# Optimization experiments

Hardware: AMD Instinct MI355X
Metric: run time of the kernel (lower is better)

Reference implementation:

```python
import jax, jax.numpy as jnp
import numpy as np

NEI_SIZE = [16]  # matches init kwarg nei_size

def setup_inputs() -> dict:
    key = jax.random.key(0)
    k = jax.random.split(key, 5)
    B, N, S = 512, 32, 16
    EF, NF = 64, 128
    return {
        "x": jax.random.normal(k[0], (B, N, NF), dtype=jnp.float32),
        "x_nei_rel": jax.random.normal(k[1], (B, N * S, EF), dtype=jnp.float32),
        "x_nei_node": jax.random.normal(k[2], (B, N * S, NF), dtype=jnp.float32),
        "W1_w": jax.random.normal(k[3], (NF, EF + NF), dtype=jnp.float32) * 0.05,
        "W1_b": jax.random.normal(k[4], (NF,), dtype=jnp.float32) * 0.05,
        "i": 0,
    }

def reference(x, x_nei_rel, x_nei_node, W1_w, W1_b, i):
    S = NEI_SIZE[i]                       # now_nei_size (static python int)
    B, N, D = x.shape                     # N = n_neibor, D = nodeFea
    norm = 1.0 / np.sqrt(D).astype(np.float32)
    # concat edge+node feats and project: [B, N*S, EF+NF] -> [B, N*S, D]
    x_nei = jnp.concatenate([x_nei_rel, x_nei_node], axis=-1)
    v = (x_nei @ W1_w.T + W1_b).reshape(B, N, S, D)
    # per-node attention over its S neighbors
    alpha = jnp.einsum('bnd,bnsd->bns', x, v) * norm   # [B, N, S]
    alpha = jax.nn.softmax(alpha, axis=-1)
    # weighted neighbor sum
    return jnp.einsum('bns,bnsd->bnd', alpha, v)       # [B, N, D]
```

## Files before the change

### kernel.cpp

```cpp
#include <hip/hip_runtime.h>
#include <stdint.h>


typedef __attribute__((ext_vector_type(8))) short short8;
typedef __attribute__((ext_vector_type(4))) float float4_t;
typedef __attribute__((ext_vector_type(4))) unsigned short ushort4_t;

#define GRID_ 1024
#define ITERS_ 16

__device__ __forceinline__ unsigned short f2bf(float f) {
    uint32_t u = __float_as_uint(f);
    u += 0x7fffu + ((u >> 16) & 1u);
    return (unsigned short)(u >> 16);
}

__device__ __forceinline__ int aoff(int s, int kc) {
    return (((kc >> 5) * 64) + (((kc & 31) >> 3) * 16) + s) * 8 + (kc & 7);
}

__global__ __launch_bounds__(256) void nei_attn_kernel(
    const float* __restrict__ x,
    const float* __restrict__ rel,
    const float* __restrict__ node,
    const float* __restrict__ W,
    const float* __restrict__ bias,
    float* __restrict__ out)
{
    __shared__ __align__(16) unsigned short lds_a[6 * 64 * 8];
    __shared__ float lds_x[128];
    __shared__ float lds_v[16 * 132];
    __shared__ float lds_ap[256];
    __shared__ float lds_alpha[16];

    const int t    = threadIdx.x;
    const int lane = t & 63;
    const int wv   = t >> 6;
    const int l15  = lane & 15;
    const int quad = lane >> 4;

    short8 bf0[6], bf1[6];
    const int row0 = wv * 32 + l15;
    const int row1 = row0 + 16;
    const float bias0 = bias[row0];
    const float bias1 = bias[row1];
    #pragma unroll
    for (int q = 0; q < 6; ++q) {
        const float* p0 = W + row0 * 192 + q * 32 + quad * 8;
        const float* p1 = W + row1 * 192 + q * 32 + quad * 8;
        float4_t a0 = *(const float4_t*)p0;
        float4_t a1 = *(const float4_t*)(p0 + 4);
        float4_t c0 = *(const float4_t*)p1;
        float4_t c1 = *(const float4_t*)(p1 + 4);
        short8 f0, f1;
        f0[0] = (short)f2bf(a0.x); f0[1] = (short)f2bf(a0.y);
        f0[2] = (short)f2bf(a0.z); f0[3] = (short)f2bf(a0.w);
        f0[4] = (short)f2bf(a1.x); f0[5] = (short)f2bf(a1.y);
        f0[6] = (short)f2bf(a1.z); f0[7] = (short)f2bf(a1.w);
        f1[0] = (short)f2bf(c0.x); f1[1] = (short)f2bf(c0.y);
        f1[2] = (short)f2bf(c0.z); f1[3] = (short)f2bf(c0.w);
        f1[4] = (short)f2bf(c1.x); f1[5] = (short)f2bf(c1.y);
        f1[6] = (short)f2bf(c1.z); f1[7] = (short)f2bf(c1.w);
        bf0[q] = f0; bf1[q] = f1;
    }

    const int s0 = t >> 4,       kc0 = (t & 15) << 2;
    const int s1 = t >> 5,       kc1 = 64 + ((t & 31) << 2);
    const int s2 = s1 + 8;
    const int ao0 = aoff(s0, kc0);
    const int ao1 = aoff(s1, kc1);
    const int ao2 = aoff(s2, kc1);

    int idx = blockIdx.x * ITERS_;

    float4_t pf0, pf1, pf2, pfx;
    {
        const float* pr = rel  + idx * 1024;
        const float* pn = node + idx * 2048;
        pf0 = *(const float4_t*)(pr + t * 4);
        pf1 = *(const float4_t*)(pn + t * 4);
        pf2 = *(const float4_t*)(pn + 1024 + t * 4);
        if (t < 32) pfx = *(const float4_t*)(x + idx * 128 + t * 4);
    }

    for (int it = 0; it < ITERS_; ++it) {
        {
            ushort4_t u;
            u[0] = f2bf(pf0.x); u[1] = f2bf(pf0.y); u[2] = f2bf(pf0.z); u[3] = f2bf(pf0.w);
            *(ushort4_t*)&lds_a[ao0] = u;
            u[0] = f2bf(pf1.x); u[1] = f2bf(pf1.y); u[2] = f2bf(pf1.z); u[3] = f2bf(pf1.w);
            *(ushort4_t*)&lds_a[ao1] = u;
            u[0] = f2bf(pf2.x); u[1] = f2bf(pf2.y); u[2] = f2bf(pf2.z); u[3] = f2bf(pf2.w);
            *(ushort4_t*)&lds_a[ao2] = u;
            if (t < 32) *(float4_t*)&lds_x[t * 4] = pfx;
        }
        __syncthreads();

        if (it + 1 < ITERS_) {
            const int nidx = idx + 1;
            const float* pr = rel  + nidx * 1024;
            const float* pn = node + nidx * 2048;
            pf0 = *(const float4_t*)(pr + t * 4);
            pf1 = *(const float4_t*)(pn + t * 4);
            pf2 = *(const float4_t*)(pn + 1024 + t * 4);
            if (t < 32) pfx = *(const float4_t*)(x + nidx * 128 + t * 4);
        }

        float4_t acc0 = {0.f, 0.f, 0.f, 0.f};
        float4_t acc1 = {0.f, 0.f, 0.f, 0.f};
        #pragma unroll
        for (int q = 0; q < 6; ++q) {
            short8 af = *(const short8*)&lds_a[(q * 64 + lane) * 8];
            acc0 = __builtin_amdgcn_mfma_f32_16x16x32_bf16(af, bf0[q], acc0, 0, 0, 0);
            acc1 = __builtin_amdgcn_mfma_f32_16x16x32_bf16(af, bf1[q], acc1, 0, 0, 0);
        }

        const int col0 = wv * 32 + l15;
        const int rb = quad * 4;
        #pragma unroll
        for (int r = 0; r < 4; ++r) {
            lds_v[(rb + r) * 132 + col0]      = acc0[r] + bias0;
            lds_v[(rb + r) * 132 + col0 + 16] = acc1[r] + bias1;
        }
        __syncthreads();

        {
            const int sA = t >> 4, dA = t & 15;
            float p = 0.f;
            #pragma unroll
            for (int j = 0; j < 8; ++j) {
                const int d = dA + (j << 4);
                p += lds_x[d] * lds_v[sA * 132 + d];
            }
            lds_ap[t] = p;
        }
        __syncthreads();

        if (t < 16) {
            float a = 0.f;
            #pragma unroll
            for (int j = 0; j < 16; ++j) a += lds_ap[t * 16 + j];
            lds_alpha[t] = a * 0.08838834764831845f;
        }
        __syncthreads();

        if (t < 128) {
            float m = lds_alpha[0];
            #pragma unroll
            for (int s = 1; s < 16; ++s) m = fmaxf(m, lds_alpha[s]);
            float e[16], den = 0.f;
            #pragma unroll
            for (int s = 0; s < 16; ++s) { e[s] = __expf(lds_alpha[s] - m); den += e[s]; }
            float o = 0.f;
            #pragma unroll
            for (int s = 0; s < 16; ++s) o += e[s] * lds_v[s * 132 + t];
            out[idx * 128 + t] = o / den;
        }
        ++idx;
    }
}

extern "C" void kernel_launch(void* const* d_in, const int* in_sizes, int n_in,
                              void* d_out, int out_size, void* d_ws, size_t ws_size,
                              hipStream_t stream) {
    const float* x    = (const float*)d_in[0];
    const float* rel  = (const float*)d_in[1];
    const float* node = (const float*)d_in[2];
    const float* W    = (const float*)d_in[3];
    const float* bias = (const float*)d_in[4];
    float* out = (float*)d_out;
    hipLaunchKernelGGL(nei_attn_kernel, dim3(GRID_), dim3(256), 0, stream,
                       x, rel, node, W, bias, out);
}
```

Measured before the change: 263.0 us.

## Give each wave its own node tile with W staged in LDS and shuffle softmax

Restructures the kernel so each of four waves independently processes whole (b,n) tiles: the full bf16 weight matrix is staged once in LDS and shared across waves. Each wave computes all 128 output columns with MFMA and does the attention dot product, softmax and weighted sum entirely in registers via cross-lane shuffles. This removes the per-iteration block-wide __syncthreads barriers and LDS round trips for v, alpha and partial sums. Grid and iterations change to 512 blocks x 4 waves x 8 tiles, with launch bounds hinting two blocks per CU. Costs are roughly 48KB of LDS per block, more LDS reads of W per tile and heavier register use for the prefetch buffers.

```diff
diff --git a/kernel.cpp b/kernel.cpp
--- a/kernel.cpp
+++ b/kernel.cpp
@@ -6,8 +6,8 @@
 typedef __attribute__((ext_vector_type(4))) float float4_t;
 typedef __attribute__((ext_vector_type(4))) unsigned short ushort4_t;
 
-#define GRID_ 1024
-#define ITERS_ 16
+#define NBLK 512
+#define ITERS 8
 
 __device__ __forceinline__ unsigned short f2bf(float f) {
     uint32_t u = __float_as_uint(f);
@@ -19,7 +19,7 @@
     return (((kc >> 5) * 64) + (((kc & 31) >> 3) * 16) + s) * 8 + (kc & 7);
 }
 
-__global__ __launch_bounds__(256) void nei_attn_kernel(
+__global__ __launch_bounds__(256, 2) void nei_attn_kernel(
     const float* __restrict__ x,
     const float* __restrict__ rel,
     const float* __restrict__ node,
@@ -27,11 +27,9 @@
     const float* __restrict__ bias,
     float* __restrict__ out)
 {
-    __shared__ __align__(16) unsigned short lds_a[6 * 64 * 8];
-    __shared__ float lds_x[128];
-    __shared__ float lds_v[16 * 132];
-    __shared__ float lds_ap[256];
-    __shared__ float lds_alpha[16];
+    __shared__ __align__(16) unsigned short lds_w[48 * 64 * 8];
+    __shared__ __align__(16) unsigned short lds_a[4][6 * 64 * 8];
+    __shared__ __align__(16) float lds_x[4][128];
 
     const int t    = threadIdx.x;
     const int lane = t & 63;
@@ -39,124 +37,137 @@
     const int l15  = lane & 15;
     const int quad = lane >> 4;
 
-    short8 bf0[6], bf1[6];
-    const int row0 = wv * 32 + l15;
-    const int row1 = row0 + 16;
-    const float bias0 = bias[row0];
-    const float bias1 = bias[row1];
     #pragma unroll
-    for (int q = 0; q < 6; ++q) {
-        const float* p0 = W + row0 * 192 + q * 32 + quad * 8;
-        const float* p1 = W + row1 * 192 + q * 32 + quad * 8;
-        float4_t a0 = *(const float4_t*)p0;
-        float4_t a1 = *(const float4_t*)(p0 + 4);
-        float4_t c0 = *(const float4_t*)p1;
-        float4_t c1 = *(const float4_t*)(p1 + 4);
-        short8 f0, f1;
-        f0[0] = (short)f2bf(a0.x); f0[1] = (short)f2bf(a0.y);
-        f0[2] = (short)f2bf(a0.z); f0[3] = (short)f2bf(a0.w);
-        f0[4] = (short)f2bf(a1.x); f0[5] = (short)f2bf(a1.y);
-        f0[6] = (short)f2bf(a1.z); f0[7] = (short)f2bf(a1.w);
-        f1[0] = (short)f2bf(c0.x); f1[1] = (short)f2bf(c0.y);
-        f1[2] = (short)f2bf(c0.z); f1[3] = (short)f2bf(c0.w);
-        f1[4] = (short)f2bf(c1.x); f1[5] = (short)f2bf(c1.y);
-        f1[6] = (short)f2bf(c1.z); f1[7] = (short)f2bf(c1.w);
-        bf0[q] = f0; bf1[q] = f1;
+    for (int c = 0; c < 12; ++c) {
+        const int ch = c * 4 + wv;
+        const int ct = ch / 6, q = ch - ct * 6;
+        const float* p = W + (ct * 16 + l15) * 192 + q * 32 + quad * 8;
+        float4_t w0 = *(const float4_t*)p;
+        float4_t w1 = *(const float4_t*)(p + 4);
+        short8 f;
+        f[0] = (short)f2bf(w0.x); f[1] = (short)f2bf(w0.y);
+        f[2] = (short)f2bf(w0.z); f[3] = (short)f2bf(w0.w);
+        f[4] = (short)f2bf(w1.x); f[5] = (short)f2bf(w1.y);
+        f[6] = (short)f2bf(w1.z); f[7] = (short)f2bf(w1.w);
+        *(short8*)&lds_w[(ch * 64 + lane) * 8] = f;
+    }
+    float bias_l[8];
+    #pragma unroll
+    for (int ct = 0; ct < 8; ++ct) bias_l[ct] = bias[ct * 16 + l15];
+
+    int aor[4], aon[8];
+    #pragma unroll
+    for (int c = 0; c < 4; ++c) aor[c] = aoff(l15, (quad + 4 * c) * 4);
+    #pragma unroll
+    for (int c = 0; c < 8; ++c) aon[c] = aoff(l15, 64 + (quad + 4 * c) * 4);
+
+    __syncthreads();
+
+    int tile = (blockIdx.x * 4 + wv) * ITERS;
+
+    float4_t pr[4], pn[8], px = (float4_t){0.f, 0.f, 0.f, 0.f};
+    {
+        const float4_t* rb = (const float4_t*)(rel  + (size_t)tile * 1024);
+        const float4_t* nb = (const float4_t*)(node + (size_t)tile * 2048);
+        #pragma unroll
+        for (int c = 0; c < 4; ++c) pr[c] = rb[l15 * 16 + quad + 4 * c];
+        #pragma unroll
+        for (int c = 0; c < 8; ++c) pn[c] = nb[l15 * 32 + quad + 4 * c];
+        if (lane < 32) px = ((const float4_t*)(x + (size_t)tile * 128))[lane];
     }
 
-    const int s0 = t >> 4,       kc0 = (t & 15) << 2;
-    const int s1 = t >> 5,       kc1 = 64 + ((t & 31) << 2);
-    const int s2 = s1 + 8;
-    const int ao0 = aoff(s0, kc0);
-    const int ao1 = aoff(s1, kc1);
-    const int ao2 = aoff(s2, kc1);
+    for (int it = 0; it < ITERS; ++it) {
+        #pragma unroll
+        for (int c = 0; c < 4; ++c) {
+            ushort4_t u;
+            u[0] = f2bf(pr[c].x); u[1] = f2bf(pr[c].y);
+            u[2] = f2bf(pr[c].z); u[3] = f2bf(pr[c].w);
+            *(ushort4_t*)&lds_a[wv][aor[c]] = u;
+        }
+        #pragma unroll
+        for (int c = 0; c < 8; ++c) {
+            ushort4_t u;
+            u[0] = f2bf(pn[c].x); u[1] = f2bf(pn[c].y);
+            u[2] = f2bf(pn[c].z); u[3] = f2bf(pn[c].w);
+            *(ushort4_t*)&lds_a[wv][aon[c]] = u;
+        }
+        if (lane < 32) *(float4_t*)&lds_x[wv][lane * 4] = px;
 
-    int idx = blockIdx.x * ITERS_;
-
-    float4_t pf0, pf1, pf2, pfx;
-    {
-        const float* pr = rel  + idx * 1024;
-        const float* pn = node + idx * 2048;
-        pf0 = *(const float4_t*)(pr + t * 4);
-        pf1 = *(const float4_t*)(pn + t * 4);
-        pf2 = *(const float4_t*)(pn + 1024 + t * 4);
-        if (t < 32) pfx = *(const float4_t*)(x + idx * 128 + t * 4);
-    }
-
-    for (int it = 0; it < ITERS_; ++it) {
-        {
-            ushort4_t u;
-            u[0] = f2bf(pf0.x); u[1] = f2bf(pf0.y); u[2] = f2bf(pf0.z); u[3] = f2bf(pf0.w);
-            *(ushort4_t*)&lds_a[ao0] = u;
-            u[0] = f2bf(pf1.x); u[1] = f2bf(pf1.y); u[2] = f2bf(pf1.z); u[3] = f2bf(pf1.w);
-            *(ushort4_t*)&lds_a[ao1] = u;
-            u[0] = f2bf(pf2.x); u[1] = f2bf(pf2.y); u[2] = f2bf(pf2.z); u[3] = f2bf(pf2.w);
-            *(ushort4_t*)&lds_a[ao2] = u;
-            if (t < 32) *(float4_t*)&lds_x[t * 4] = pfx;
-        }
-        __syncthreads();
-
-        if (it + 1 < ITERS_) {
-            const int nidx = idx + 1;
-            const float* pr = rel  + nidx * 1024;
-            const float* pn = node + nidx * 2048;
-            pf0 = *(const float4_t*)(pr + t * 4);
-            pf1 = *(const float4_t*)(pn + t * 4);
-            pf2 = *(const float4_t*)(pn + 1024 + t * 4);
-            if (t < 32) pfx = *(const float4_t*)(x + nidx * 128 + t * 4);
+        if (it + 1 < ITERS) {
+            const int nt = tile + 1;
+            const float4_t* rb = (const float4_t*)(rel  + (size_t)nt * 1024);
+            const float4_t* nb = (const float4_t*)(node + (size_t)nt * 2048);
+            #pragma unroll
+            for (int c = 0; c < 4; ++c) pr[c] = rb[l15 * 16 + quad + 4 * c];
+            #pragma unroll
+            for (int c = 0; c < 8; ++c) pn[c] = nb[l15 * 32 + quad + 4 * c];
+            if (lane < 32) px = ((const float4_t*)(x + (size_t)nt * 128))[lane];
         }
 
-        float4_t acc0 = {0.f, 0.f, 0.f, 0.f};
-        float4_t acc1 = {0.f, 0.f, 0.f, 0.f};
+        short8 areg[6];
         #pragma unroll
-        for (int q = 0; q < 6; ++q) {
-            short8 af = *(const short8*)&lds_a[(q * 64 + lane) * 8];
-            acc0 = __builtin_amdgcn_mfma_f32_16x16x32_bf16(af, bf0[q], acc0, 0, 0, 0);
-            acc1 = __builtin_amdgcn_mfma_f32_16x16x32_bf16(af, bf1[q], acc1, 0, 0, 0);
+        for (int q = 0; q < 6; ++q)
+            areg[q] = *(const short8*)&lds_a[wv][(q * 64 + lane) * 8];
+
+        float4_t acc[8];
+        #pragma unroll
+        for (int ct = 0; ct < 8; ++ct) acc[ct] = (float4_t){0.f, 0.f, 0.f, 0.f};
+        #pragma unroll
+        for (int ct = 0; ct < 8; ++ct) {
+            #pragma unroll
+            for (int q = 0; q < 6; ++q) {
+                short8 b = *(const short8*)&lds_w[((ct * 6 + q) * 64 + lane) * 8];
+                acc[ct] = __builtin_amdgcn_mfma_f32_16x16x32_bf16(areg[q], b, acc[ct], 0, 0, 0);
+            }
+        }
+        #pragma unroll
+        for (int ct = 0; ct < 8; ++ct) {
+            acc[ct][0] += bias_l[ct]; acc[ct][1] += bias_l[ct];
+            acc[ct][2] += bias_l[ct]; acc[ct][3] += bias_l[ct];
         }
 
-        const int col0 = wv * 32 + l15;
-        const int rb = quad * 4;
+        float xr[8];
         #pragma unroll
-        for (int r = 0; r < 4; ++r) {
-            lds_v[(rb + r) * 132 + col0]      = acc0[r] + bias0;
-            lds_v[(rb + r) * 132 + col0 + 16] = acc1[r] + bias1;
+        for (int ct = 0; ct < 8; ++ct) xr[ct] = lds_x[wv][ct * 16 + l15];
+
+        float p0 = 0.f, p1 = 0.f, p2 = 0.f, p3 = 0.f;
+        #pragma unroll
+        for (int ct = 0; ct < 8; ++ct) {
+            p0 += xr[ct] * acc[ct][0]; p1 += xr[ct] * acc[ct][1];
+            p2 += xr[ct] * acc[ct][2]; p3 += xr[ct] * acc[ct][3];
         }
-        __syncthreads();
+        #pragma unroll
+        for (int m = 1; m <= 8; m <<= 1) {
+            p0 += __shfl_xor(p0, m); p1 += __shfl_xor(p1, m);
+            p2 += __shfl_xor(p2, m); p3 += __shfl_xor(p3, m);
+        }
+        const float norm = 0.08838834764831845f;
+        p0 *= norm; p1 *= norm; p2 *= norm; p3 *= norm;
+        float mx = fmaxf(fmaxf(p0, p1), fmaxf(p2, p3));
+        mx = fmaxf(mx, __shfl_xor(mx, 16));
+        mx = fmaxf(mx, __shfl_xor(mx, 32));
+        float e0 = __expf(p0 - mx), e1 = __expf(p1 - mx);
+        float e2 = __expf(p2 - mx), e3 = __expf(p3 - mx);
+        float den = e0 + e1 + e2 + e3;
+        den += __shfl_xor(den, 16);
+        den += __shfl_xor(den, 32);
+        const float inv = 1.0f / den;
+        const float w0 = e0 * inv, w1 = e1 * inv, w2 = e2 * inv, w3 = e3 * inv;
 
-        {
-            const int sA = t >> 4, dA = t & 15;
-            float p = 0.f;
-            #pragma unroll
-            for (int j = 0; j < 8; ++j) {
-                const int d = dA + (j << 4);
-                p += lds_x[d] * lds_v[sA * 132 + d];
-            }
-            lds_ap[t] = p;
+        float s0 = 0.f, s1 = 0.f;
+        #pragma unroll
+        for (int ct = 0; ct < 8; ++ct) {
+            float v = w0 * acc[ct][0] + w1 * acc[ct][1]
+                    + w2 * acc[ct][2] + w3 * acc[ct][3];
+            v += __shfl_xor(v, 16);
+            v += __shfl_xor(v, 32);
+            if ((ct >> 1) == quad) { if (ct & 1) s1 = v; else s0 = v; }
         }
-        __syncthreads();
+        float* ob = out + (size_t)tile * 128;
+        ob[quad * 32 + l15]      = s0;
+        ob[quad * 32 + 16 + l15] = s1;
 
-        if (t < 16) {
-            float a = 0.f;
-            #pragma unroll
-            for (int j = 0; j < 16; ++j) a += lds_ap[t * 16 + j];
-            lds_alpha[t] = a * 0.08838834764831845f;
-        }
-        __syncthreads();
-
-        if (t < 128) {
-            float m = lds_alpha[0];
-            #pragma unroll
-            for (int s = 1; s < 16; ++s) m = fmaxf(m, lds_alpha[s]);
-            float e[16], den = 0.f;
-            #pragma unroll
-            for (int s = 0; s < 16; ++s) { e[s] = __expf(lds_alpha[s] - m); den += e[s]; }
-            float o = 0.f;
-            #pragma unroll
-            for (int s = 0; s < 16; ++s) o += e[s] * lds_v[s * 132 + t];
-            out[idx * 128 + t] = o / den;
-        }
-        ++idx;
+        ++tile;
     }
 }
 
@@ -169,6 +180,6 @@
     const float* W    = (const float*)d_in[3];
     const float* bias = (const float*)d_in[4];
     float* out = (float*)d_out;
-    hipLaunchKernelGGL(nei_attn_kernel, dim3(GRID_), dim3(256), 0, stream,
+    hipLaunchKernelGGL(nei_attn_kernel, dim3(NBLK), dim3(256), 0, stream,
                        x, rel, node, W, bias, out);
 }
```

Result: slower. 291.4 us (+10.8%).

## Restructure into 2-wave blocks with shuffle softmax and deferred bias

Applied to the files above, without the earlier changes.

The kernel now runs 128-thread blocks of two waves, each wave owning 64 output features, on a larger grid with fewer tiles per block. The MFMA operands are swapped so the weights are the A fragment. The attention dot product is taken from the accumulators with cross-lane shuffles, and the 16-way softmax uses wave shuffles, cutting four barriers per tile to two. The bias is added after the weighted sum, which is valid because the softmax weights sum to one. In exchange, the explicit register prefetch of the next tile is dropped and each thread holds more weight fragments in registers.

```diff
diff --git a/kernel.cpp b/kernel.cpp
--- a/kernel.cpp
+++ b/kernel.cpp
@@ -6,8 +6,8 @@
 typedef __attribute__((ext_vector_type(4))) float float4_t;
 typedef __attribute__((ext_vector_type(4))) unsigned short ushort4_t;
 
-#define GRID_ 1024
-#define ITERS_ 16
+#define NBLK 2048
+#define TILES_PER_BLK 8
 
 __device__ __forceinline__ unsigned short f2bf(float f) {
     uint32_t u = __float_as_uint(f);
@@ -19,7 +19,7 @@
     return (((kc >> 5) * 64) + (((kc & 31) >> 3) * 16) + s) * 8 + (kc & 7);
 }
 
-__global__ __launch_bounds__(256) void nei_attn_kernel(
+__global__ __launch_bounds__(128, 3) void nei_attn_kernel(
     const float* __restrict__ x,
     const float* __restrict__ rel,
     const float* __restrict__ node,
@@ -27,11 +27,10 @@
     const float* __restrict__ bias,
     float* __restrict__ out)
 {
-    __shared__ __align__(16) unsigned short lds_a[6 * 64 * 8];
-    __shared__ float lds_x[128];
-    __shared__ float lds_v[16 * 132];
-    __shared__ float lds_ap[256];
-    __shared__ float lds_alpha[16];
+    __shared__ __align__(16) unsigned short lds_f[6 * 64 * 8];
+    __shared__ __align__(16) float lds_v[16][132];
+    __shared__ float lds_alpha[2][16];
+    __shared__ float lds_w[2][16];
 
     const int t    = threadIdx.x;
     const int lane = t & 63;
@@ -39,124 +38,111 @@
     const int l15  = lane & 15;
     const int quad = lane >> 4;
 
-    short8 bf0[6], bf1[6];
-    const int row0 = wv * 32 + l15;
-    const int row1 = row0 + 16;
-    const float bias0 = bias[row0];
-    const float bias1 = bias[row1];
+    short8 wfrag[4][6];
     #pragma unroll
-    for (int q = 0; q < 6; ++q) {
-        const float* p0 = W + row0 * 192 + q * 32 + quad * 8;
-        const float* p1 = W + row1 * 192 + q * 32 + quad * 8;
-        float4_t a0 = *(const float4_t*)p0;
-        float4_t a1 = *(const float4_t*)(p0 + 4);
-        float4_t c0 = *(const float4_t*)p1;
-        float4_t c1 = *(const float4_t*)(p1 + 4);
-        short8 f0, f1;
-        f0[0] = (short)f2bf(a0.x); f0[1] = (short)f2bf(a0.y);
-        f0[2] = (short)f2bf(a0.z); f0[3] = (short)f2bf(a0.w);
-        f0[4] = (short)f2bf(a1.x); f0[5] = (short)f2bf(a1.y);
-        f0[6] = (short)f2bf(a1.z); f0[7] = (short)f2bf(a1.w);
-        f1[0] = (short)f2bf(c0.x); f1[1] = (short)f2bf(c0.y);
-        f1[2] = (short)f2bf(c0.z); f1[3] = (short)f2bf(c0.w);
-        f1[4] = (short)f2bf(c1.x); f1[5] = (short)f2bf(c1.y);
-        f1[6] = (short)f2bf(c1.z); f1[7] = (short)f2bf(c1.w);
-        bf0[q] = f0; bf1[q] = f1;
+    for (int dt = 0; dt < 4; ++dt) {
+        const float* wr = W + (size_t)(64 * wv + dt * 16 + l15) * 192;
+        #pragma unroll
+        for (int q = 0; q < 6; ++q) {
+            const float* p = wr + q * 32 + quad * 8;
+            float4_t a = *(const float4_t*)p;
+            float4_t b = *(const float4_t*)(p + 4);
+            short8 f;
+            f[0] = (short)f2bf(a.x); f[1] = (short)f2bf(a.y);
+            f[2] = (short)f2bf(a.z); f[3] = (short)f2bf(a.w);
+            f[4] = (short)f2bf(b.x); f[5] = (short)f2bf(b.y);
+            f[6] = (short)f2bf(b.z); f[7] = (short)f2bf(b.w);
+            wfrag[dt][q] = f;
+        }
     }
+    const float bias_l = bias[64 * wv + lane];
 
-    const int s0 = t >> 4,       kc0 = (t & 15) << 2;
-    const int s1 = t >> 5,       kc1 = 64 + ((t & 31) << 2);
-    const int s2 = s1 + 8;
-    const int ao0 = aoff(s0, kc0);
-    const int ao1 = aoff(s1, kc1);
-    const int ao2 = aoff(s2, kc1);
+    const int s_st = wv * 8 + (lane & 7);
+    const int fb   = lane >> 3;
+    int ao[6];
+    #pragma unroll
+    for (int c = 0; c < 6; ++c) ao[c] = aoff(s_st, (fb + 8 * c) * 4);
 
-    int idx = blockIdx.x * ITERS_;
-
-    float4_t pf0, pf1, pf2, pfx;
-    {
-        const float* pr = rel  + idx * 1024;
-        const float* pn = node + idx * 2048;
-        pf0 = *(const float4_t*)(pr + t * 4);
-        pf1 = *(const float4_t*)(pn + t * 4);
-        pf2 = *(const float4_t*)(pn + 1024 + t * 4);
-        if (t < 32) pfx = *(const float4_t*)(x + idx * 128 + t * 4);
-    }
-
-    for (int it = 0; it < ITERS_; ++it) {
+    int tile = blockIdx.x * TILES_PER_BLK;
+    for (int it = 0; it < TILES_PER_BLK; ++it, ++tile) {
+        float4_t ld[6];
         {
+            const float4_t* rb = (const float4_t*)rel  + (size_t)tile * 256 + s_st * 16;
+            const float4_t* nb = (const float4_t*)node + (size_t)tile * 512 + s_st * 32;
+            ld[0] = rb[fb];      ld[1] = rb[fb + 8];
+            ld[2] = nb[fb];      ld[3] = nb[fb + 8];
+            ld[4] = nb[fb + 16]; ld[5] = nb[fb + 24];
+        }
+        #pragma unroll
+        for (int c = 0; c < 6; ++c) {
             ushort4_t u;
-            u[0] = f2bf(pf0.x); u[1] = f2bf(pf0.y); u[2] = f2bf(pf0.z); u[3] = f2bf(pf0.w);
-            *(ushort4_t*)&lds_a[ao0] = u;
-            u[0] = f2bf(pf1.x); u[1] = f2bf(pf1.y); u[2] = f2bf(pf1.z); u[3] = f2bf(pf1.w);
-            *(ushort4_t*)&lds_a[ao1] = u;
-            u[0] = f2bf(pf2.x); u[1] = f2bf(pf2.y); u[2] = f2bf(pf2.z); u[3] = f2bf(pf2.w);
-            *(ushort4_t*)&lds_a[ao2] = u;
-            if (t < 32) *(float4_t*)&lds_x[t * 4] = pfx;
+            u[0] = f2bf(ld[c].x); u[1] = f2bf(ld[c].y);
+            u[2] = f2bf(ld[c].z); u[3] = f2bf(ld[c].w);
+            *(ushort4_t*)&lds_f[ao[c]] = u;
         }
         __syncthreads();
 
-        if (it + 1 < ITERS_) {
-            const int nidx = idx + 1;
-            const float* pr = rel  + nidx * 1024;
-            const float* pn = node + nidx * 2048;
-            pf0 = *(const float4_t*)(pr + t * 4);
-            pf1 = *(const float4_t*)(pn + t * 4);
-            pf2 = *(const float4_t*)(pn + 1024 + t * 4);
-            if (t < 32) pfx = *(const float4_t*)(x + nidx * 128 + t * 4);
+        float4_t xv[4];
+        #pragma unroll
+        for (int dt = 0; dt < 4; ++dt)
+            xv[dt] = *(const float4_t*)(x + (size_t)tile * 128 + 64 * wv + 16 * dt + 4 * quad);
+
+        float4_t acc[4];
+        #pragma unroll
+        for (int dt = 0; dt < 4; ++dt) acc[dt] = (float4_t){0.f, 0.f, 0.f, 0.f};
+        #pragma unroll
+        for (int q = 0; q < 6; ++q) {
+            short8 bfr = *(const short8*)&lds_f[(q * 64 + lane) * 8];
+            #pragma unroll
+            for (int dt = 0; dt < 4; ++dt)
+                acc[dt] = __builtin_amdgcn_mfma_f32_16x16x32_bf16(wfrag[dt][q], bfr, acc[dt], 0, 0, 0);
         }
 
-        float4_t acc0 = {0.f, 0.f, 0.f, 0.f};
-        float4_t acc1 = {0.f, 0.f, 0.f, 0.f};
+        float ap = 0.f;
         #pragma unroll
-        for (int q = 0; q < 6; ++q) {
-            short8 af = *(const short8*)&lds_a[(q * 64 + lane) * 8];
-            acc0 = __builtin_amdgcn_mfma_f32_16x16x32_bf16(af, bf0[q], acc0, 0, 0, 0);
-            acc1 = __builtin_amdgcn_mfma_f32_16x16x32_bf16(af, bf1[q], acc1, 0, 0, 0);
-        }
+        for (int dt = 0; dt < 4; ++dt)
+            ap += xv[dt].x * acc[dt][0] + xv[dt].y * acc[dt][1]
+                + xv[dt].z * acc[dt][2] + xv[dt].w * acc[dt][3];
+        ap += __shfl_xor(ap, 16);
+        ap += __shfl_xor(ap, 32);
+        if (lane < 16) lds_alpha[wv][lane] = ap;
 
-        const int col0 = wv * 32 + l15;
-        const int rb = quad * 4;
         #pragma unroll
-        for (int r = 0; r < 4; ++r) {
-            lds_v[(rb + r) * 132 + col0]      = acc0[r] + bias0;
-            lds_v[(rb + r) * 132 + col0 + 16] = acc1[r] + bias1;
-        }
+        for (int dt = 0; dt < 4; ++dt)
+            *(float4_t*)&lds_v[l15][64 * wv + 16 * dt + 4 * quad] = acc[dt];
+
         __syncthreads();
 
-        {
-            const int sA = t >> 4, dA = t & 15;
-            float p = 0.f;
-            #pragma unroll
-            for (int j = 0; j < 8; ++j) {
-                const int d = dA + (j << 4);
-                p += lds_x[d] * lds_v[sA * 132 + d];
-            }
-            lds_ap[t] = p;
-        }
-        __syncthreads();
+        const float alpha = (ap + lds_alpha[1 - wv][l15]) * 0.08838834764831845f;
+        float mx = alpha;
+        mx = fmaxf(mx, __shfl_xor(mx, 1));
+        mx = fmaxf(mx, __shfl_xor(mx, 2));
+        mx = fmaxf(mx, __shfl_xor(mx, 4));
+        mx = fmaxf(mx, __shfl_xor(mx, 8));
+        const float e = __expf(alpha - mx);
+        float den = e;
+        den += __shfl_xor(den, 1);
+        den += __shfl_xor(den, 2);
+        den += __shfl_xor(den, 4);
+        den += __shfl_xor(den, 8);
+        const float wgt = e / den;
+        if (quad == 0) lds_w[wv][l15] = wgt;
 
-        if (t < 16) {
-            float a = 0.f;
-            #pragma unroll
-            for (int j = 0; j < 16; ++j) a += lds_ap[t * 16 + j];
-            lds_alpha[t] = a * 0.08838834764831845f;
-        }
-        __syncthreads();
-
-        if (t < 128) {
-            float m = lds_alpha[0];
-            #pragma unroll
-            for (int s = 1; s < 16; ++s) m = fmaxf(m, lds_alpha[s]);
-            float e[16], den = 0.f;
-            #pragma unroll
-            for (int s = 0; s < 16; ++s) { e[s] = __expf(lds_alpha[s] - m); den += e[s]; }
-            float o = 0.f;
-            #pragma unroll
-            for (int s = 0; s < 16; ++s) o += e[s] * lds_v[s * 132 + t];
-            out[idx * 128 + t] = o / den;
-        }
-        ++idx;
+        const int md = 64 * wv + lane;
+        float4_t w0 = *(const float4_t*)&lds_w[wv][0];
+        float4_t w1 = *(const float4_t*)&lds_w[wv][4];
+        float4_t w2 = *(const float4_t*)&lds_w[wv][8];
+        float4_t w3 = *(const float4_t*)&lds_w[wv][12];
+        float o = bias_l;
+        o += w0.x * lds_v[0][md]  + w0.y * lds_v[1][md]
+           + w0.z * lds_v[2][md]  + w0.w * lds_v[3][md];
+        o += w1.x * lds_v[4][md]  + w1.y * lds_v[5][md]
+           + w1.z * lds_v[6][md]  + w1.w * lds_v[7][md];
+        o += w2.x * lds_v[8][md]  + w2.y * lds_v[9][md]
+           + w2.z * lds_v[10][md] + w2.w * lds_v[11][md];
+        o += w3.x * lds_v[12][md] + w3.y * lds_v[13][md]
+           + w3.z * lds_v[14][md] + w3.w * lds_v[15][md];
+        out[(size_t)tile * 128 + md] = o;
     }
 }
 
@@ -169,6 +155,6 @@
     const float* W    = (const float*)d_in[3];
     const float* bias = (const float*)d_in[4];
     float* out = (float*)d_out;
-    hipLaunchKernelGGL(nei_attn_kernel, dim3(GRID_), dim3(256), 0, stream,
+    hipLaunchKernelGGL(nei_attn_kernel, dim3(NBLK), dim3(128), 0, stream,
                        x, rel, node, W, bias, out);
 }
```

New measurement: 299.7 us. 1.14x slower.
